# Performance work log

Hardware: AMD Instinct MI355X
Metric: run time of the kernel (lower is better)

## Reference

```python
import jax, jax.numpy as jnp
import numpy as np

N = 50000      # nodes
E = 1_000_000  # edges (avg degree 20)
D = 64         # hidden dim
L = 3          # num dynamics layers
LN_EPS = 1e-5


def layernorm(h, g, b):
    mu = jnp.mean(h, axis=-1, keepdims=True)
    var = jnp.mean(jnp.square(h - mu), axis=-1, keepdims=True)
    return (h - mu) * jax.lax.rsqrt(var + LN_EPS) * g + b


def transformer_conv(h, src, dst, Wq, bq, Wk, bk, Wv, bv, Ws, bs):
    # PyG TransformerConv, heads=1, concat=False, beta=False, root_weight=True
    n = h.shape[0]
    d = Wq.shape[1]
    q = h @ Wq + bq            # [N, D] queries (dst side)
    k = h @ Wk + bk            # [N, D] keys   (src side)
    v = h @ Wv + bv            # [N, D] values (src side)
    logits = jnp.sum(q[dst] * k[src], axis=-1) / jnp.sqrt(jnp.asarray(d, h.dtype))  # [E]
    # segment softmax over incoming edges of each dst node
    m = jax.ops.segment_max(logits, dst, num_segments=n)      # [N]
    e = jnp.exp(logits - m[dst])                               # [E]
    s = jax.ops.segment_sum(e, dst, num_segments=n)            # [N]
    a = e / s[dst]                                             # [E]
    agg = jax.ops.segment_sum(a[:, None] * v[src], dst, num_segments=n)  # [N, D]
    return agg + h @ Ws + bs   # root/skip connection


def setup_inputs() -> dict:
    key = jax.random.key(0)
    ks = jax.random.split(key, 24)
    w = lambda k, shape: (jax.random.normal(k, shape, jnp.float32) * 0.05)
    inp = {
        "x": jax.random.normal(ks[0], (N, D), jnp.float32),
        "edge_index": jax.random.randint(ks[1], (2, E), 0, N, jnp.int32),
        # input_proj conv params
        "Wq0": w(ks[2], (D, D)), "bq0": w(ks[3], (D,)),
        "Wk0": w(ks[4], (D, D)), "bk0": w(ks[5], (D,)),
        "Wv0": w(ks[6], (D, D)), "bv0": w(ks[7], (D,)),
        "Ws0": w(ks[8], (D, D)), "bs0": w(ks[9], (D,)),
        "ln0_g": jnp.ones((D,), jnp.float32), "ln0_b": jnp.zeros((D,), jnp.float32),
        # stacked dynamics conv params [L, ...]
        "Wq": w(ks[10], (L, D, D)), "bq": w(ks[11], (L, D)),
        "Wk": w(ks[12], (L, D, D)), "bk": w(ks[13], (L, D)),
        "Wv": w(ks[14], (L, D, D)), "bv": w(ks[15], (L, D)),
        "Ws": w(ks[16], (L, D, D)), "bs": w(ks[17], (L, D)),
        "ln_g": jnp.ones((L, D), jnp.float32), "ln_b": jnp.zeros((L, D), jnp.float32),
    }
    return inp


def reference(x, edge_index, Wq0, bq0, Wk0, bk0, Wv0, bv0, Ws0, bs0, ln0_g, ln0_b,
              Wq, bq, Wk, bk, Wv, bv, Ws, bs, ln_g, ln_b):
    src, dst = edge_index[0], edge_index[1]
    h = transformer_conv(x, src, dst, Wq0, bq0, Wk0, bk0, Wv0, bv0, Ws0, bs0)
    h = jax.nn.relu(layernorm(h, ln0_g, ln0_b))
    # dropout is identity in eval mode
    for i in range(L):
        hi = transformer_conv(h, src, dst, Wq[i], bq[i], Wk[i], bk[i],
                              Wv[i], bv[i], Ws[i], bs[i])
        h = jax.nn.relu(layernorm(hi + h, ln_g[i], ln_b[i]))
    return h
```

## Files before the change

kernel.cpp:

```cpp
#include <hip/hip_runtime.h>
#include <math.h>

#define NN 50000
#define NE 1000000
#define CAP 64
#define LN_EPS 1e-5f
#define ROW_TILES 3125
#define GEMM_BLOCKS 782
#define BE_T 250112
#define ELL_BLOCKS 977

typedef __attribute__((ext_vector_type(8))) short short8;
typedef __attribute__((ext_vector_type(8))) unsigned short ushort8;
typedef __attribute__((ext_vector_type(4))) float f32x4;

__device__ __forceinline__ unsigned short f2bf(float f) {
  union { float f; unsigned u; } v; v.f = f;
  unsigned r = v.u + 0x7FFF + ((v.u >> 16) & 1);
  return (unsigned short)(r >> 16);
}
__device__ __forceinline__ float bf2f(unsigned short b) {
  union { unsigned u; float f; } v; v.u = ((unsigned)b) << 16;
  return v.f;
}

__global__ __launch_bounds__(256) void wprep(
    const float* __restrict__ Wq0, const float* __restrict__ bq0,
    const float* __restrict__ Wk0, const float* __restrict__ bk0,
    const float* __restrict__ Wv0, const float* __restrict__ bv0,
    const float* __restrict__ Ws0, const float* __restrict__ bs0,
    const float* __restrict__ WqL, const float* __restrict__ bqL,
    const float* __restrict__ WkL, const float* __restrict__ bkL,
    const float* __restrict__ WvL, const float* __restrict__ bvL,
    const float* __restrict__ WsL, const float* __restrict__ bsL,
    unsigned short* __restrict__ Wt, float* __restrict__ Bc) {
  int tid = blockIdx.x * 256 + threadIdx.x;
  if (tid >= 4 * 256 * 64) return;
  int lyr = tid >> 14;
  int rem = tid & 16383;
  int c = rem >> 6;
  int k = rem & 63;
  int m = c >> 6;
  int n = c & 63;
  const float *W, *B;
  if (lyr == 0) {
    const float* Wm[4] = {Wq0, Wk0, Wv0, Ws0};
    const float* Bm[4] = {bq0, bk0, bv0, bs0};
    W = Wm[m]; B = Bm[m];
  } else {
    const float* Wm[4] = {WqL, WkL, WvL, WsL};
    const float* Bm[4] = {bqL, bkL, bvL, bsL};
    W = Wm[m] + (size_t)(lyr - 1) * 4096;
    B = Bm[m] + (size_t)(lyr - 1) * 64;
  }
  Wt[(size_t)lyr * 16384 + (size_t)c * 64 + k] = f2bf(W[(size_t)k * 64 + n]);
  if (k == 0) Bc[lyr * 256 + c] = B[n];
}

__global__ __launch_bounds__(256) void gemm_qkvs(
    const float* __restrict__ h, const unsigned short* __restrict__ Wt,
    const float* __restrict__ Bc, unsigned short* __restrict__ Qb,
    unsigned int* __restrict__ KVb, float* __restrict__ Sf,
    const int* __restrict__ ei, int* __restrict__ cursor,
    unsigned short* __restrict__ ell, int nGemm) {
  __shared__ unsigned short lw[256 * 72];
  int tid = threadIdx.x;

  if ((int)blockIdx.x >= nGemm) {
    int t = (blockIdx.x - nGemm) * 256 + tid;
    int e[4]; bool v[4]; int s[4], d[4], p[4];
#pragma unroll
    for (int i = 0; i < 4; ++i) { e[i] = t + i * BE_T; v[i] = e[i] < NE; }
#pragma unroll
    for (int i = 0; i < 4; ++i) {
      if (v[i]) { s[i] = ei[e[i]]; d[i] = ei[NE + e[i]]; }
    }
#pragma unroll
    for (int i = 0; i < 4; ++i) {
      if (v[i]) p[i] = atomicAdd(&cursor[d[i]], 1);
    }
#pragma unroll
    for (int i = 0; i < 4; ++i) {
      if (v[i] && p[i] < CAP) ell[(size_t)d[i] * CAP + p[i]] = (unsigned short)s[i];
    }
    return;
  }

#pragma unroll
  for (int it = 0; it < 8; ++it) {
    int id = it * 256 + tid;
    int row = id >> 3, cc = id & 7;
    float4 src = *reinterpret_cast<const float4*>(Wt + (size_t)row * 64 + cc * 8);
    *reinterpret_cast<float4*>(lw + (size_t)row * 72 + cc * 8) = src;
  }
  __syncthreads();

  int wave = tid >> 6, lane = tid & 63;
  int tile = blockIdx.x * 4 + wave;
  if (tile >= ROW_TILES) return;
  int lo = lane & 15, hi = lane >> 4;
  int row = tile * 16 + lo;
  const float* hrow = h + (size_t)row * 64;

  auto packA = [&](const float* p) {
    float4 x = *reinterpret_cast<const float4*>(p);
    float4 y = *reinterpret_cast<const float4*>(p + 4);
    short8 r;
    r[0] = (short)f2bf(x.x); r[1] = (short)f2bf(x.y);
    r[2] = (short)f2bf(x.z); r[3] = (short)f2bf(x.w);
    r[4] = (short)f2bf(y.x); r[5] = (short)f2bf(y.y);
    r[6] = (short)f2bf(y.z); r[7] = (short)f2bf(y.w);
    return r;
  };
  short8 a0 = packA(hrow + hi * 8);
  short8 a1 = packA(hrow + 32 + hi * 8);

  int rb = tile * 16 + hi * 4;

  auto mm = [&](int brow, float bias) {
    f32x4 acc = {bias, bias, bias, bias};
    const unsigned short* wr = lw + (size_t)brow * 72 + hi * 8;
    short8 b0 = *reinterpret_cast<const short8*>(wr);
    short8 b1 = *reinterpret_cast<const short8*>(wr + 32);
    acc = __builtin_amdgcn_mfma_f32_16x16x32_bf16(a0, b0, acc, 0, 0, 0);
    acc = __builtin_amdgcn_mfma_f32_16x16x32_bf16(a1, b1, acc, 0, 0, 0);
    return acc;
  };

#pragma unroll
  for (int ct = 0; ct < 4; ++ct) {
    int col = ct * 16 + lo;
    f32x4 acc = mm(col, Bc[col]);
#pragma unroll
    for (int r = 0; r < 4; ++r) Qb[(size_t)(rb + r) * 64 + col] = f2bf(acc[r]);
  }
#pragma unroll
  for (int cg = 0; cg < 4; ++cg) {
    int col = cg * 16 + lo;
    f32x4 aK = mm(64 + col, Bc[64 + col]);
    f32x4 aV = mm(128 + col, Bc[128 + col]);
#pragma unroll
    for (int r = 0; r < 4; ++r) {
      unsigned int pk = (unsigned int)f2bf(aK[r]) | ((unsigned int)f2bf(aV[r]) << 16);
      KVb[(size_t)(rb + r) * 64 + col] = pk;
    }
  }
#pragma unroll
  for (int ct = 0; ct < 4; ++ct) {
    int col = ct * 16 + lo;
    f32x4 acc = mm(192 + col, Bc[192 + col]);
#pragma unroll
    for (int r = 0; r < 4; ++r) Sf[(size_t)(rb + r) * 64 + col] = acc[r];
  }
}

__global__ __launch_bounds__(256) void edge_fused(
    const unsigned short* __restrict__ Qb, const unsigned short* __restrict__ KVb,
    const float* __restrict__ Sf,
    const unsigned short* __restrict__ ell, const int* __restrict__ cursor,
    const float* __restrict__ ln_g, const float* __restrict__ ln_b,
    const float* __restrict__ h_res, float* __restrict__ h_out, int use_res) {
  int node = blockIdx.x * 4 + (threadIdx.x >> 6);
  if (node >= NN) return;
  int lane = threadIdx.x & 63;
  int g = lane >> 4, t = lane & 15;

  int deg = cursor[node];
  if (deg > CAP) deg = CAP;
  const unsigned short* lst = ell + (size_t)node * CAP;

  ushort4 qv = *reinterpret_cast<const ushort4*>(Qb + (size_t)node * 64 + t * 4);
  float q0 = bf2f(qv.x), q1 = bf2f(qv.y), q2 = bf2f(qv.z), q3 = bf2f(qv.w);

  int passes = (deg + 3) >> 2;

  auto ldkv = [&](int p) {
    int slot = p * 4 + g;
    int src = (slot < deg) ? (int)lst[slot] : 0;
    return *reinterpret_cast<const ushort8*>(KVb + (size_t)src * 128 + t * 8);
  };

  float4 acc = {0.f, 0.f, 0.f, 0.f};
  float ssum = 0.f;
  ushort8 b0 = ldkv(0);
  ushort8 b1 = ldkv(1);
  for (int p = 0; p < passes; ++p) {
    ushort8 b2 = ldkv(p + 2);
    bool valid = (p * 4 + g) < deg;
    float dp = q0 * bf2f(b0[0]) + q1 * bf2f(b0[2]) +
               q2 * bf2f(b0[4]) + q3 * bf2f(b0[6]);
    dp += __shfl_xor(dp, 1, 64);
    dp += __shfl_xor(dp, 2, 64);
    dp += __shfl_xor(dp, 4, 64);
    dp += __shfl_xor(dp, 8, 64);
    float w = valid ? __expf(dp * 0.125f) : 0.f;
    ssum += w;
    acc.x = fmaf(w, bf2f(b0[1]), acc.x);
    acc.y = fmaf(w, bf2f(b0[3]), acc.y);
    acc.z = fmaf(w, bf2f(b0[5]), acc.z);
    acc.w = fmaf(w, bf2f(b0[7]), acc.w);
    b0 = b1; b1 = b2;
  }
#pragma unroll
  for (int off = 16; off <= 32; off <<= 1) {
    acc.x += __shfl_xor(acc.x, off, 64);
    acc.y += __shfl_xor(acc.y, off, 64);
    acc.z += __shfl_xor(acc.z, off, 64);
    acc.w += __shfl_xor(acc.w, off, 64);
    ssum  += __shfl_xor(ssum, off, 64);
  }
  float inv = (ssum > 0.f) ? (1.f / ssum) : 0.f;

  float4 s4 = *reinterpret_cast<const float4*>(Sf + (size_t)node * 64 + t * 4);
  float4 o;
  o.x = acc.x * inv + s4.x;
  o.y = acc.y * inv + s4.y;
  o.z = acc.z * inv + s4.z;
  o.w = acc.w * inv + s4.w;
  if (use_res) {
    float4 r4 = *reinterpret_cast<const float4*>(h_res + (size_t)node * 64 + t * 4);
    o.x += r4.x; o.y += r4.y; o.z += r4.z; o.w += r4.w;
  }

  float sum = o.x + o.y + o.z + o.w;
  sum += __shfl_xor(sum, 1, 64);
  sum += __shfl_xor(sum, 2, 64);
  sum += __shfl_xor(sum, 4, 64);
  sum += __shfl_xor(sum, 8, 64);
  float mu = sum * (1.f / 64.f);
  float dx = o.x - mu, dy = o.y - mu, dz = o.z - mu, dw = o.w - mu;
  float vs = dx * dx + dy * dy + dz * dz + dw * dw;
  vs += __shfl_xor(vs, 1, 64);
  vs += __shfl_xor(vs, 2, 64);
  vs += __shfl_xor(vs, 4, 64);
  vs += __shfl_xor(vs, 8, 64);
  float rstd = rsqrtf(vs * (1.f / 64.f) + LN_EPS);
  float4 gg = *reinterpret_cast<const float4*>(ln_g + t * 4);
  float4 bb = *reinterpret_cast<const float4*>(ln_b + t * 4);
  float4 y;
  y.x = fmaxf(dx * rstd * gg.x + bb.x, 0.f);
  y.y = fmaxf(dy * rstd * gg.y + bb.y, 0.f);
  y.z = fmaxf(dz * rstd * gg.z + bb.z, 0.f);
  y.w = fmaxf(dw * rstd * gg.w + bb.w, 0.f);
  *reinterpret_cast<float4*>(h_out + (size_t)node * 64 + t * 4) = y;
}

extern "C" void kernel_launch(void* const* d_in, const int* in_sizes, int n_in,
                              void* d_out, int out_size, void* d_ws, size_t ws_size,
                              hipStream_t stream) {
  const float* x    = (const float*)d_in[0];
  const int*   ei   = (const int*)d_in[1];
  const float* Wq0  = (const float*)d_in[2];
  const float* bq0  = (const float*)d_in[3];
  const float* Wk0  = (const float*)d_in[4];
  const float* bk0  = (const float*)d_in[5];
  const float* Wv0  = (const float*)d_in[6];
  const float* bv0  = (const float*)d_in[7];
  const float* Ws0  = (const float*)d_in[8];
  const float* bs0  = (const float*)d_in[9];
  const float* ln0g = (const float*)d_in[10];
  const float* ln0b = (const float*)d_in[11];
  const float* WqL  = (const float*)d_in[12];
  const float* bqL  = (const float*)d_in[13];
  const float* WkL  = (const float*)d_in[14];
  const float* bkL  = (const float*)d_in[15];
  const float* WvL  = (const float*)d_in[16];
  const float* bvL  = (const float*)d_in[17];
  const float* WsL  = (const float*)d_in[18];
  const float* bsL  = (const float*)d_in[19];
  const float* lnG  = (const float*)d_in[20];
  const float* lnB  = (const float*)d_in[21];

  float* h = (float*)d_out;

  char* ws = (char*)d_ws;
  size_t off = 0;
  unsigned short* Qb = (unsigned short*)(ws + off);  off += (size_t)NN * 64 * 2;
  float* Sf = (float*)(ws + off);                    off += (size_t)NN * 64 * 4;
  unsigned int* KVb = (unsigned int*)(ws + off);     off += (size_t)NN * 128 * 2;
  unsigned short* ell = (unsigned short*)(ws + off); off += (size_t)NN * CAP * 2;
  int* cursor = (int*)(ws + off);                    off += (size_t)NN * 4;
  unsigned short* Wt = (unsigned short*)(ws + off);  off += (size_t)4 * 256 * 64 * 2;
  float* Bc = (float*)(ws + off);                    off += (size_t)4 * 256 * 4;

  hipMemsetAsync(cursor, 0, NN * sizeof(int), stream);
  wprep<<<256, 256, 0, stream>>>(Wq0, bq0, Wk0, bk0, Wv0, bv0, Ws0, bs0,
                                 WqL, bqL, WkL, bkL, WvL, bvL, WsL, bsL, Wt, Bc);

  for (int layer = 0; layer < 4; ++layer) {
    const float* hin = (layer == 0) ? x : h;
    const float* lg = (layer == 0) ? ln0g : lnG + (size_t)(layer - 1) * 64;
    const float* lb = (layer == 0) ? ln0b : lnB + (size_t)(layer - 1) * 64;
    int extra = (layer == 0) ? ELL_BLOCKS : 0;
    gemm_qkvs<<<GEMM_BLOCKS + extra, 256, 0, stream>>>(
        hin, Wt + (size_t)layer * 16384, Bc + (size_t)layer * 256,
        Qb, KVb, Sf, ei, cursor, ell, GEMM_BLOCKS);
    edge_fused<<<(NN + 3) / 4, 256, 0, stream>>>(
        Qb, (const unsigned short*)KVb, Sf, ell, cursor, lg, lb, h, h,
        layer > 0 ? 1 : 0);
  }
}
```

Baseline: 392.5 us.

## Split K/V buffers, process eight edges per pass, fold cursor reset into wprep

The edge kernel now maps eight lanes per edge and eight edges per pass, reading K and V from separate bf16 arrays. This halves the number of serial passes per node and shortens the dot-product shuffle reduction, and each lane now holds eight accumulators. The cursor memset is folded into the weight-prep kernel to remove one launch. The ELL list is widened to 32-bit entries written with atomicExch, which doubles its footprint and turns plain stores into atomics.

```diff
diff --git a/kernel.cpp b/kernel.cpp
--- a/kernel.cpp
+++ b/kernel.cpp
@@ -33,8 +33,10 @@
     const float* __restrict__ WkL, const float* __restrict__ bkL,
     const float* __restrict__ WvL, const float* __restrict__ bvL,
     const float* __restrict__ WsL, const float* __restrict__ bsL,
-    unsigned short* __restrict__ Wt, float* __restrict__ Bc) {
+    unsigned short* __restrict__ Wt, float* __restrict__ Bc,
+    int* __restrict__ cursor) {
   int tid = blockIdx.x * 256 + threadIdx.x;
+  if (tid < NN) cursor[tid] = 0;
   if (tid >= 4 * 256 * 64) return;
   int lyr = tid >> 14;
   int rem = tid & 16383;
@@ -60,9 +62,10 @@
 __global__ __launch_bounds__(256) void gemm_qkvs(
     const float* __restrict__ h, const unsigned short* __restrict__ Wt,
     const float* __restrict__ Bc, unsigned short* __restrict__ Qb,
-    unsigned int* __restrict__ KVb, float* __restrict__ Sf,
+    unsigned short* __restrict__ Kb, unsigned short* __restrict__ Vb,
+    float* __restrict__ Sf,
     const int* __restrict__ ei, int* __restrict__ cursor,
-    unsigned short* __restrict__ ell, int nGemm) {
+    unsigned int* __restrict__ ell, int nGemm) {
   __shared__ unsigned short lw[256 * 72];
   int tid = threadIdx.x;
 
@@ -81,7 +84,8 @@
     }
 #pragma unroll
     for (int i = 0; i < 4; ++i) {
-      if (v[i] && p[i] < CAP) ell[(size_t)d[i] * CAP + p[i]] = (unsigned short)s[i];
+      if (v[i] && p[i] < CAP)
+        atomicExch(&ell[(size_t)d[i] * CAP + p[i]], (unsigned int)s[i]);
     }
     return;
   }
@@ -135,15 +139,18 @@
     for (int r = 0; r < 4; ++r) Qb[(size_t)(rb + r) * 64 + col] = f2bf(acc[r]);
   }
 #pragma unroll
-  for (int cg = 0; cg < 4; ++cg) {
-    int col = cg * 16 + lo;
-    f32x4 aK = mm(64 + col, Bc[64 + col]);
-    f32x4 aV = mm(128 + col, Bc[128 + col]);
-#pragma unroll
-    for (int r = 0; r < 4; ++r) {
-      unsigned int pk = (unsigned int)f2bf(aK[r]) | ((unsigned int)f2bf(aV[r]) << 16);
-      KVb[(size_t)(rb + r) * 64 + col] = pk;
-    }
+  for (int ct = 0; ct < 4; ++ct) {
+    int col = ct * 16 + lo;
+    f32x4 acc = mm(64 + col, Bc[64 + col]);
+#pragma unroll
+    for (int r = 0; r < 4; ++r) Kb[(size_t)(rb + r) * 64 + col] = f2bf(acc[r]);
+  }
+#pragma unroll
+  for (int ct = 0; ct < 4; ++ct) {
+    int col = ct * 16 + lo;
+    f32x4 acc = mm(128 + col, Bc[128 + col]);
+#pragma unroll
+    for (int r = 0; r < 4; ++r) Vb[(size_t)(rb + r) * 64 + col] = f2bf(acc[r]);
   }
 #pragma unroll
   for (int ct = 0; ct < 4; ++ct) {
@@ -155,94 +162,95 @@
 }
 
 __global__ __launch_bounds__(256) void edge_fused(
-    const unsigned short* __restrict__ Qb, const unsigned short* __restrict__ KVb,
-    const float* __restrict__ Sf,
-    const unsigned short* __restrict__ ell, const int* __restrict__ cursor,
+    const unsigned short* __restrict__ Qb, const unsigned short* __restrict__ Kb,
+    const unsigned short* __restrict__ Vb, const float* __restrict__ Sf,
+    const unsigned int* __restrict__ ell, const int* __restrict__ cursor,
     const float* __restrict__ ln_g, const float* __restrict__ ln_b,
     const float* __restrict__ h_res, float* __restrict__ h_out, int use_res) {
   int node = blockIdx.x * 4 + (threadIdx.x >> 6);
   if (node >= NN) return;
   int lane = threadIdx.x & 63;
-  int g = lane >> 4, t = lane & 15;
+  int e = lane >> 3, d = lane & 7;
 
   int deg = cursor[node];
   if (deg > CAP) deg = CAP;
-  const unsigned short* lst = ell + (size_t)node * CAP;
-
-  ushort4 qv = *reinterpret_cast<const ushort4*>(Qb + (size_t)node * 64 + t * 4);
-  float q0 = bf2f(qv.x), q1 = bf2f(qv.y), q2 = bf2f(qv.z), q3 = bf2f(qv.w);
-
-  int passes = (deg + 3) >> 2;
-
-  auto ldkv = [&](int p) {
-    int slot = p * 4 + g;
+  const unsigned int* lst = ell + (size_t)node * CAP;
+
+  ushort8 q8 = *reinterpret_cast<const ushort8*>(Qb + (size_t)node * 64 + d * 8);
+  float q[8];
+#pragma unroll
+  for (int j = 0; j < 8; ++j) q[j] = bf2f(q8[j]);
+
+  int passes = (deg + 7) >> 3;
+
+  auto ld8 = [&](int p, const unsigned short* T) {
+    int slot = p * 8 + e;
     int src = (slot < deg) ? (int)lst[slot] : 0;
-    return *reinterpret_cast<const ushort8*>(KVb + (size_t)src * 128 + t * 8);
+    return *reinterpret_cast<const ushort8*>(T + (size_t)src * 64 + d * 8);
   };
 
-  float4 acc = {0.f, 0.f, 0.f, 0.f};
+  float acc[8] = {0.f, 0.f, 0.f, 0.f, 0.f, 0.f, 0.f, 0.f};
   float ssum = 0.f;
-  ushort8 b0 = ldkv(0);
-  ushort8 b1 = ldkv(1);
+  ushort8 k0 = ld8(0, Kb), v0 = ld8(0, Vb);
+  ushort8 k1 = ld8(1, Kb), v1 = ld8(1, Vb);
   for (int p = 0; p < passes; ++p) {
-    ushort8 b2 = ldkv(p + 2);
-    bool valid = (p * 4 + g) < deg;
-    float dp = q0 * bf2f(b0[0]) + q1 * bf2f(b0[2]) +
-               q2 * bf2f(b0[4]) + q3 * bf2f(b0[6]);
+    ushort8 k2 = ld8(p + 2, Kb), v2 = ld8(p + 2, Vb);
+    bool valid = (p * 8 + e) < deg;
+    float dp = 0.f;
+#pragma unroll
+    for (int j = 0; j < 8; ++j) dp += q[j] * bf2f(k0[j]);
     dp += __shfl_xor(dp, 1, 64);
     dp += __shfl_xor(dp, 2, 64);
     dp += __shfl_xor(dp, 4, 64);
-    dp += __shfl_xor(dp, 8, 64);
     float w = valid ? __expf(dp * 0.125f) : 0.f;
     ssum += w;
-    acc.x = fmaf(w, bf2f(b0[1]), acc.x);
-    acc.y = fmaf(w, bf2f(b0[3]), acc.y);
-    acc.z = fmaf(w, bf2f(b0[5]), acc.z);
-    acc.w = fmaf(w, bf2f(b0[7]), acc.w);
-    b0 = b1; b1 = b2;
-  }
-#pragma unroll
-  for (int off = 16; off <= 32; off <<= 1) {
-    acc.x += __shfl_xor(acc.x, off, 64);
-    acc.y += __shfl_xor(acc.y, off, 64);
-    acc.z += __shfl_xor(acc.z, off, 64);
-    acc.w += __shfl_xor(acc.w, off, 64);
-    ssum  += __shfl_xor(ssum, off, 64);
+#pragma unroll
+    for (int j = 0; j < 8; ++j) acc[j] = fmaf(w, bf2f(v0[j]), acc[j]);
+    k0 = k1; v0 = v1; k1 = k2; v1 = v2;
+  }
+#pragma unroll
+  for (int off = 8; off <= 32; off <<= 1) {
+#pragma unroll
+    for (int j = 0; j < 8; ++j) acc[j] += __shfl_xor(acc[j], off, 64);
+    ssum += __shfl_xor(ssum, off, 64);
   }
   float inv = (ssum > 0.f) ? (1.f / ssum) : 0.f;
 
-  float4 s4 = *reinterpret_cast<const float4*>(Sf + (size_t)node * 64 + t * 4);
-  float4 o;
-  o.x = acc.x * inv + s4.x;
-  o.y = acc.y * inv + s4.y;
-  o.z = acc.z * inv + s4.z;
-  o.w = acc.w * inv + s4.w;
+  const float* sp = Sf + (size_t)node * 64 + d * 8;
+  float o[8];
+#pragma unroll
+  for (int j = 0; j < 8; ++j) o[j] = acc[j] * inv + sp[j];
   if (use_res) {
-    float4 r4 = *reinterpret_cast<const float4*>(h_res + (size_t)node * 64 + t * 4);
-    o.x += r4.x; o.y += r4.y; o.z += r4.z; o.w += r4.w;
-  }
-
-  float sum = o.x + o.y + o.z + o.w;
+    const float* rp = h_res + (size_t)node * 64 + d * 8;
+#pragma unroll
+    for (int j = 0; j < 8; ++j) o[j] += rp[j];
+  }
+
+  float sum = 0.f;
+#pragma unroll
+  for (int j = 0; j < 8; ++j) sum += o[j];
   sum += __shfl_xor(sum, 1, 64);
   sum += __shfl_xor(sum, 2, 64);
   sum += __shfl_xor(sum, 4, 64);
-  sum += __shfl_xor(sum, 8, 64);
   float mu = sum * (1.f / 64.f);
-  float dx = o.x - mu, dy = o.y - mu, dz = o.z - mu, dw = o.w - mu;
-  float vs = dx * dx + dy * dy + dz * dz + dw * dw;
+  float vs = 0.f;
+#pragma unroll
+  for (int j = 0; j < 8; ++j) { float t = o[j] - mu; vs += t * t; }
   vs += __shfl_xor(vs, 1, 64);
   vs += __shfl_xor(vs, 2, 64);
   vs += __shfl_xor(vs, 4, 64);
-  vs += __shfl_xor(vs, 8, 64);
   float rstd = rsqrtf(vs * (1.f / 64.f) + LN_EPS);
-  float4 gg = *reinterpret_cast<const float4*>(ln_g + t * 4);
-  float4 bb = *reinterpret_cast<const float4*>(ln_b + t * 4);
-  float4 y;
-  y.x = fmaxf(dx * rstd * gg.x + bb.x, 0.f);
-  y.y = fmaxf(dy * rstd * gg.y + bb.y, 0.f);
-  y.z = fmaxf(dz * rstd * gg.z + bb.z, 0.f);
-  y.w = fmaxf(dw * rstd * gg.w + bb.w, 0.f);
-  *reinterpret_cast<float4*>(h_out + (size_t)node * 64 + t * 4) = y;
+  if (e == 0) {
+    const float* gp = ln_g + d * 8;
+    const float* bp = ln_b + d * 8;
+    float y[8];
+#pragma unroll
+    for (int j = 0; j < 8; ++j)
+      y[j] = fmaxf((o[j] - mu) * rstd * gp[j] + bp[j], 0.f);
+    float* op = h_out + (size_t)node * 64 + d * 8;
+    *reinterpret_cast<float4*>(op) = make_float4(y[0], y[1], y[2], y[3]);
+    *reinterpret_cast<float4*>(op + 4) = make_float4(y[4], y[5], y[6], y[7]);
+  }
 }
 
 extern "C" void kernel_launch(void* const* d_in, const int* in_sizes, int n_in,
@@ -276,16 +284,17 @@
   char* ws = (char*)d_ws;
   size_t off = 0;
   unsigned short* Qb = (unsigned short*)(ws + off);  off += (size_t)NN * 64 * 2;
+  unsigned short* Kb = (unsigned short*)(ws + off);  off += (size_t)NN * 64 * 2;
+  unsigned short* Vb = (unsigned short*)(ws + off);  off += (size_t)NN * 64 * 2;
   float* Sf = (float*)(ws + off);                    off += (size_t)NN * 64 * 4;
-  unsigned int* KVb = (unsigned int*)(ws + off);     off += (size_t)NN * 128 * 2;
-  unsigned short* ell = (unsigned short*)(ws + off); off += (size_t)NN * CAP * 2;
+  unsigned int* ell = (unsigned int*)(ws + off);     off += (size_t)NN * CAP * 4;
   int* cursor = (int*)(ws + off);                    off += (size_t)NN * 4;
   unsigned short* Wt = (unsigned short*)(ws + off);  off += (size_t)4 * 256 * 64 * 2;
   float* Bc = (float*)(ws + off);                    off += (size_t)4 * 256 * 4;
 
-  hipMemsetAsync(cursor, 0, NN * sizeof(int), stream);
   wprep<<<256, 256, 0, stream>>>(Wq0, bq0, Wk0, bk0, Wv0, bv0, Ws0, bs0,
-                                 WqL, bqL, WkL, bkL, WvL, bvL, WsL, bsL, Wt, Bc);
+                                 WqL, bqL, WkL, bkL, WvL, bvL, WsL, bsL,
+                                 Wt, Bc, cursor);
 
   for (int layer = 0; layer < 4; ++layer) {
     const float* hin = (layer == 0) ? x : h;
@@ -294,9 +303,8 @@
     int extra = (layer == 0) ? ELL_BLOCKS : 0;
     gemm_qkvs<<<GEMM_BLOCKS + extra, 256, 0, stream>>>(
         hin, Wt + (size_t)layer * 16384, Bc + (size_t)layer * 256,
-        Qb, KVb, Sf, ei, cursor, ell, GEMM_BLOCKS);
+        Qb, Kb, Vb, Sf, ei, cursor, ell, GEMM_BLOCKS);
     edge_fused<<<(NN + 3) / 4, 256, 0, stream>>>(
-        Qb, (const unsigned short*)KVb, Sf, ell, cursor, lg, lb, h, h,
-        layer > 0 ? 1 : 0);
-  }
-}
+        Qb, Kb, Vb, Sf, ell, cursor, lg, lb, h, h, layer > 0 ? 1 : 0);
+  }
+}
```

Result: slower. 424.0 us (+8.0%).

## Store keys in FP8, split K/V buffers, transpose MFMA for vectorized stores

Applied to the files above, without the earlier changes.

Keys are now stored as FP8 (4 bytes per lane chunk) in a separate buffer from bf16 values, which cuts the gather bytes per edge in the edge kernel. The 1/sqrt(d) scale is folded into Q at GEMM time. The MFMA operands are swapped so each lane owns contiguous output columns, allowing vectorized row stores. The gather prefetch depth goes from 2 to 3, the cursor memset is folded into the weight-prep kernel, and redundant output stores by 3 of 4 lane groups are removed. FP8 keys lower attention-logit precision, which risks accuracy loss.

```diff
diff --git a/kernel.cpp b/kernel.cpp
--- a/kernel.cpp
+++ b/kernel.cpp
@@ -13,6 +13,7 @@
 typedef __attribute__((ext_vector_type(8))) short short8;
 typedef __attribute__((ext_vector_type(8))) unsigned short ushort8;
 typedef __attribute__((ext_vector_type(4))) float f32x4;
+typedef __attribute__((ext_vector_type(2))) float f32x2;
 
 __device__ __forceinline__ unsigned short f2bf(float f) {
   union { float f; unsigned u; } v; v.f = f;
@@ -33,8 +34,10 @@
     const float* __restrict__ WkL, const float* __restrict__ bkL,
     const float* __restrict__ WvL, const float* __restrict__ bvL,
     const float* __restrict__ WsL, const float* __restrict__ bsL,
-    unsigned short* __restrict__ Wt, float* __restrict__ Bc) {
+    unsigned short* __restrict__ Wt, float* __restrict__ Bc,
+    int* __restrict__ cursor) {
   int tid = blockIdx.x * 256 + threadIdx.x;
+  if (tid < NN) cursor[tid] = 0;
   if (tid >= 4 * 256 * 64) return;
   int lyr = tid >> 14;
   int rem = tid & 16383;
@@ -60,7 +63,8 @@
 __global__ __launch_bounds__(256) void gemm_qkvs(
     const float* __restrict__ h, const unsigned short* __restrict__ Wt,
     const float* __restrict__ Bc, unsigned short* __restrict__ Qb,
-    unsigned int* __restrict__ KVb, float* __restrict__ Sf,
+    unsigned int* __restrict__ K8, unsigned short* __restrict__ Vb,
+    float* __restrict__ Sf,
     const int* __restrict__ ei, int* __restrict__ cursor,
     unsigned short* __restrict__ ell, int nGemm) {
   __shared__ unsigned short lw[256 * 72];
@@ -99,8 +103,8 @@
   int tile = blockIdx.x * 4 + wave;
   if (tile >= ROW_TILES) return;
   int lo = lane & 15, hi = lane >> 4;
-  int row = tile * 16 + lo;
-  const float* hrow = h + (size_t)row * 64;
+  int node = tile * 16 + lo;
+  const float* hrow = h + (size_t)node * 64;
 
   auto packA = [&](const float* p) {
     float4 x = *reinterpret_cast<const float4*>(p);
@@ -115,48 +119,49 @@
   short8 a0 = packA(hrow + hi * 8);
   short8 a1 = packA(hrow + 32 + hi * 8);
 
-  int rb = tile * 16 + hi * 4;
-
-  auto mm = [&](int brow, float bias) {
-    f32x4 acc = {bias, bias, bias, bias};
+  auto mm = [&](int brow, f32x4 bias4) {
+    f32x4 acc = bias4;
     const unsigned short* wr = lw + (size_t)brow * 72 + hi * 8;
     short8 b0 = *reinterpret_cast<const short8*>(wr);
     short8 b1 = *reinterpret_cast<const short8*>(wr + 32);
-    acc = __builtin_amdgcn_mfma_f32_16x16x32_bf16(a0, b0, acc, 0, 0, 0);
-    acc = __builtin_amdgcn_mfma_f32_16x16x32_bf16(a1, b1, acc, 0, 0, 0);
+    acc = __builtin_amdgcn_mfma_f32_16x16x32_bf16(b0, a0, acc, 0, 0, 0);
+    acc = __builtin_amdgcn_mfma_f32_16x16x32_bf16(b1, a1, acc, 0, 0, 0);
     return acc;
   };
 
 #pragma unroll
   for (int ct = 0; ct < 4; ++ct) {
-    int col = ct * 16 + lo;
-    f32x4 acc = mm(col, Bc[col]);
-#pragma unroll
-    for (int r = 0; r < 4; ++r) Qb[(size_t)(rb + r) * 64 + col] = f2bf(acc[r]);
-  }
-#pragma unroll
-  for (int cg = 0; cg < 4; ++cg) {
-    int col = cg * 16 + lo;
-    f32x4 aK = mm(64 + col, Bc[64 + col]);
-    f32x4 aV = mm(128 + col, Bc[128 + col]);
-#pragma unroll
-    for (int r = 0; r < 4; ++r) {
-      unsigned int pk = (unsigned int)f2bf(aK[r]) | ((unsigned int)f2bf(aV[r]) << 16);
-      KVb[(size_t)(rb + r) * 64 + col] = pk;
-    }
-  }
-#pragma unroll
-  for (int ct = 0; ct < 4; ++ct) {
-    int col = ct * 16 + lo;
-    f32x4 acc = mm(192 + col, Bc[192 + col]);
-#pragma unroll
-    for (int r = 0; r < 4; ++r) Sf[(size_t)(rb + r) * 64 + col] = acc[r];
+    int c0 = ct * 16 + hi * 4;
+    f32x4 bQ = *reinterpret_cast<const f32x4*>(Bc + c0);
+    f32x4 bK = *reinterpret_cast<const f32x4*>(Bc + 64 + c0);
+    f32x4 bV = *reinterpret_cast<const f32x4*>(Bc + 128 + c0);
+    f32x4 bS = *reinterpret_cast<const f32x4*>(Bc + 192 + c0);
+    f32x4 aQ = mm(ct * 16 + lo, bQ);
+    f32x4 aK = mm(64 + ct * 16 + lo, bK);
+    f32x4 aV = mm(128 + ct * 16 + lo, bV);
+    f32x4 aS = mm(192 + ct * 16 + lo, bS);
+
+    ushort4 qs;
+    qs.x = f2bf(aQ[0] * 0.125f); qs.y = f2bf(aQ[1] * 0.125f);
+    qs.z = f2bf(aQ[2] * 0.125f); qs.w = f2bf(aQ[3] * 0.125f);
+    *reinterpret_cast<ushort4*>(Qb + (size_t)node * 64 + c0) = qs;
+
+    unsigned kq = (unsigned)__builtin_amdgcn_cvt_pk_fp8_f32(aK[0], aK[1], 0, 0);
+    kq = (unsigned)__builtin_amdgcn_cvt_pk_fp8_f32(aK[2], aK[3], (int)kq, 1);
+    K8[(size_t)node * 16 + ct * 4 + hi] = kq;
+
+    ushort4 vs4;
+    vs4.x = f2bf(aV[0]); vs4.y = f2bf(aV[1]);
+    vs4.z = f2bf(aV[2]); vs4.w = f2bf(aV[3]);
+    *reinterpret_cast<ushort4*>(Vb + (size_t)node * 64 + c0) = vs4;
+
+    *reinterpret_cast<f32x4*>(Sf + (size_t)node * 64 + c0) = aS;
   }
 }
 
 __global__ __launch_bounds__(256) void edge_fused(
-    const unsigned short* __restrict__ Qb, const unsigned short* __restrict__ KVb,
-    const float* __restrict__ Sf,
+    const unsigned short* __restrict__ Qb, const unsigned int* __restrict__ K8,
+    const unsigned short* __restrict__ Vb, const float* __restrict__ Sf,
     const unsigned short* __restrict__ ell, const int* __restrict__ cursor,
     const float* __restrict__ ln_g, const float* __restrict__ ln_b,
     const float* __restrict__ h_res, float* __restrict__ h_out, int use_res) {
@@ -174,49 +179,56 @@
 
   int passes = (deg + 3) >> 2;
 
-  auto ldkv = [&](int p) {
+  auto ldsrc = [&](int p) {
     int slot = p * 4 + g;
-    int src = (slot < deg) ? (int)lst[slot] : 0;
-    return *reinterpret_cast<const ushort8*>(KVb + (size_t)src * 128 + t * 8);
+    return (slot < deg) ? (int)lst[slot] : 0;
   };
 
-  float4 acc = {0.f, 0.f, 0.f, 0.f};
+  f32x4 acc = {0.f, 0.f, 0.f, 0.f};
   float ssum = 0.f;
-  ushort8 b0 = ldkv(0);
-  ushort8 b1 = ldkv(1);
+  int s0 = ldsrc(0), s1 = ldsrc(1), s2 = ldsrc(2);
+  unsigned k0 = K8[(size_t)s0 * 16 + t];
+  ushort4  v0 = *reinterpret_cast<const ushort4*>(Vb + (size_t)s0 * 64 + t * 4);
+  unsigned k1 = K8[(size_t)s1 * 16 + t];
+  ushort4  v1 = *reinterpret_cast<const ushort4*>(Vb + (size_t)s1 * 64 + t * 4);
+  unsigned k2 = K8[(size_t)s2 * 16 + t];
+  ushort4  v2 = *reinterpret_cast<const ushort4*>(Vb + (size_t)s2 * 64 + t * 4);
   for (int p = 0; p < passes; ++p) {
-    ushort8 b2 = ldkv(p + 2);
+    int s3 = ldsrc(p + 3);
+    unsigned k3 = K8[(size_t)s3 * 16 + t];
+    ushort4  v3 = *reinterpret_cast<const ushort4*>(Vb + (size_t)s3 * 64 + t * 4);
     bool valid = (p * 4 + g) < deg;
-    float dp = q0 * bf2f(b0[0]) + q1 * bf2f(b0[2]) +
-               q2 * bf2f(b0[4]) + q3 * bf2f(b0[6]);
+    f32x2 kA = __builtin_amdgcn_cvt_pk_f32_fp8((int)k0, 0);
+    f32x2 kB = __builtin_amdgcn_cvt_pk_f32_fp8((int)k0, 1);
+    float dp = q0 * kA.x + q1 * kA.y + q2 * kB.x + q3 * kB.y;
     dp += __shfl_xor(dp, 1, 64);
     dp += __shfl_xor(dp, 2, 64);
     dp += __shfl_xor(dp, 4, 64);
     dp += __shfl_xor(dp, 8, 64);
-    float w = valid ? __expf(dp * 0.125f) : 0.f;
+    float w = valid ? __expf(dp) : 0.f;
     ssum += w;
-    acc.x = fmaf(w, bf2f(b0[1]), acc.x);
-    acc.y = fmaf(w, bf2f(b0[3]), acc.y);
-    acc.z = fmaf(w, bf2f(b0[5]), acc.z);
-    acc.w = fmaf(w, bf2f(b0[7]), acc.w);
-    b0 = b1; b1 = b2;
+    acc[0] = fmaf(w, bf2f(v0.x), acc[0]);
+    acc[1] = fmaf(w, bf2f(v0.y), acc[1]);
+    acc[2] = fmaf(w, bf2f(v0.z), acc[2]);
+    acc[3] = fmaf(w, bf2f(v0.w), acc[3]);
+    k0 = k1; v0 = v1; k1 = k2; v1 = v2; k2 = k3; v2 = v3;
   }
 #pragma unroll
   for (int off = 16; off <= 32; off <<= 1) {
-    acc.x += __shfl_xor(acc.x, off, 64);
-    acc.y += __shfl_xor(acc.y, off, 64);
-    acc.z += __shfl_xor(acc.z, off, 64);
-    acc.w += __shfl_xor(acc.w, off, 64);
-    ssum  += __shfl_xor(ssum, off, 64);
+    acc[0] += __shfl_xor(acc[0], off, 64);
+    acc[1] += __shfl_xor(acc[1], off, 64);
+    acc[2] += __shfl_xor(acc[2], off, 64);
+    acc[3] += __shfl_xor(acc[3], off, 64);
+    ssum   += __shfl_xor(ssum, off, 64);
   }
   float inv = (ssum > 0.f) ? (1.f / ssum) : 0.f;
 
   float4 s4 = *reinterpret_cast<const float4*>(Sf + (size_t)node * 64 + t * 4);
   float4 o;
-  o.x = acc.x * inv + s4.x;
-  o.y = acc.y * inv + s4.y;
-  o.z = acc.z * inv + s4.z;
-  o.w = acc.w * inv + s4.w;
+  o.x = acc[0] * inv + s4.x;
+  o.y = acc[1] * inv + s4.y;
+  o.z = acc[2] * inv + s4.z;
+  o.w = acc[3] * inv + s4.w;
   if (use_res) {
     float4 r4 = *reinterpret_cast<const float4*>(h_res + (size_t)node * 64 + t * 4);
     o.x += r4.x; o.y += r4.y; o.z += r4.z; o.w += r4.w;
@@ -235,14 +247,16 @@
   vs += __shfl_xor(vs, 4, 64);
   vs += __shfl_xor(vs, 8, 64);
   float rstd = rsqrtf(vs * (1.f / 64.f) + LN_EPS);
-  float4 gg = *reinterpret_cast<const float4*>(ln_g + t * 4);
-  float4 bb = *reinterpret_cast<const float4*>(ln_b + t * 4);
-  float4 y;
-  y.x = fmaxf(dx * rstd * gg.x + bb.x, 0.f);
-  y.y = fmaxf(dy * rstd * gg.y + bb.y, 0.f);
-  y.z = fmaxf(dz * rstd * gg.z + bb.z, 0.f);
-  y.w = fmaxf(dw * rstd * gg.w + bb.w, 0.f);
-  *reinterpret_cast<float4*>(h_out + (size_t)node * 64 + t * 4) = y;
+  if (g == 0) {
+    float4 gg = *reinterpret_cast<const float4*>(ln_g + t * 4);
+    float4 bb = *reinterpret_cast<const float4*>(ln_b + t * 4);
+    float4 y;
+    y.x = fmaxf(dx * rstd * gg.x + bb.x, 0.f);
+    y.y = fmaxf(dy * rstd * gg.y + bb.y, 0.f);
+    y.z = fmaxf(dz * rstd * gg.z + bb.z, 0.f);
+    y.w = fmaxf(dw * rstd * gg.w + bb.w, 0.f);
+    *reinterpret_cast<float4*>(h_out + (size_t)node * 64 + t * 4) = y;
+  }
 }
 
 extern "C" void kernel_launch(void* const* d_in, const int* in_sizes, int n_in,
@@ -276,16 +290,17 @@
   char* ws = (char*)d_ws;
   size_t off = 0;
   unsigned short* Qb = (unsigned short*)(ws + off);  off += (size_t)NN * 64 * 2;
+  unsigned int* K8 = (unsigned int*)(ws + off);      off += (size_t)NN * 16 * 4;
+  unsigned short* Vb = (unsigned short*)(ws + off);  off += (size_t)NN * 64 * 2;
   float* Sf = (float*)(ws + off);                    off += (size_t)NN * 64 * 4;
-  unsigned int* KVb = (unsigned int*)(ws + off);     off += (size_t)NN * 128 * 2;
   unsigned short* ell = (unsigned short*)(ws + off); off += (size_t)NN * CAP * 2;
   int* cursor = (int*)(ws + off);                    off += (size_t)NN * 4;
   unsigned short* Wt = (unsigned short*)(ws + off);  off += (size_t)4 * 256 * 64 * 2;
   float* Bc = (float*)(ws + off);                    off += (size_t)4 * 256 * 4;
 
-  hipMemsetAsync(cursor, 0, NN * sizeof(int), stream);
   wprep<<<256, 256, 0, stream>>>(Wq0, bq0, Wk0, bk0, Wv0, bv0, Ws0, bs0,
-                                 WqL, bqL, WkL, bkL, WvL, bvL, WsL, bsL, Wt, Bc);
+                                 WqL, bqL, WkL, bkL, WvL, bvL, WsL, bsL,
+                                 Wt, Bc, cursor);
 
   for (int layer = 0; layer < 4; ++layer) {
     const float* hin = (layer == 0) ? x : h;
@@ -294,9 +309,8 @@
     int extra = (layer == 0) ? ELL_BLOCKS : 0;
     gemm_qkvs<<<GEMM_BLOCKS + extra, 256, 0, stream>>>(
         hin, Wt + (size_t)layer * 16384, Bc + (size_t)layer * 256,
-        Qb, KVb, Sf, ei, cursor, ell, GEMM_BLOCKS);
+        Qb, K8, Vb, Sf, ei, cursor, ell, GEMM_BLOCKS);
     edge_fused<<<(NN + 3) / 4, 256, 0, stream>>>(
-        Qb, (const unsigned short*)KVb, Sf, ell, cursor, lg, lb, h, h,
-        layer > 0 ? 1 : 0);
-  }
-}
+        Qb, K8, Vb, Sf, ell, cursor, lg, lb, h, h, layer > 0 ? 1 : 0);
+  }
+}
```

New measurement: 422.9 us. 1.08x slower.
